# Kernel tuning notes

Hardware: AMD Instinct MI355X
Metric: run time of the kernel (lower is better)

Reference implementation:

```python
import jax, jax.numpy as jnp
import numpy as np

T, B, DIN, DH, DOUT = 512, 256, 128, 512, 128


def setup_inputs() -> dict:
    key = jax.random.key(0)
    k1, k2, k3, k4 = jax.random.split(key, 4)
    xs = jax.random.normal(k1, (T, B, DIN), dtype=jnp.float32)
    W1x = 0.1 * jax.random.normal(k2, (DIN, DH), dtype=jnp.float32)
    # random orthogonal init for the recurrent weight, as in the original
    q, _ = jnp.linalg.qr(jax.random.normal(k3, (DH, DH), dtype=jnp.float32))
    W1h = q.astype(jnp.float32)
    b1 = jnp.zeros([], dtype=jnp.float32)
    W2 = 0.1 * jax.random.normal(k4, (DH, DOUT), dtype=jnp.float32)
    b2 = jnp.zeros([], dtype=jnp.float32)
    return {"xs": xs, "W1x": W1x, "W1h": W1h, "b1": b1, "W2": W2, "b2": b2}


def reference(xs, W1x, W1h, b1, W2, b2):
    # Precompute all input projections in one big GEMM: [T, B, DH]
    xproj = jnp.einsum('tbi,ih->tbh', xs, W1x)
    h0 = jnp.zeros((xs.shape[1], W1h.shape[0]), dtype=xs.dtype)

    def step(h, xp):
        h_new = jnp.tanh(xp + h @ W1h + b1)
        return h_new, None

    h_final, _ = jax.lax.scan(step, h0, xproj)
    return h_final @ W2 + b2
```

## Files before the change

### kernel.cpp

```cpp
#include <hip/hip_runtime.h>

#define T_STEPS 512
#define BATCH   256
#define DIN     128
#define DH      512
#define DOUT    128
#define RGRP    16

typedef __attribute__((ext_vector_type(8))) short  short8;
typedef __attribute__((ext_vector_type(4))) float  floatx4;
typedef __attribute__((ext_vector_type(4))) unsigned short ushort4v;

union Pack8 { short8 s; unsigned short h[8]; };

__device__ __forceinline__ float bf2f(unsigned short u) {
    union { unsigned int i; float f; } v; v.i = ((unsigned int)u) << 16; return v.f;
}
__device__ __forceinline__ unsigned short f2bf(float f) {
    union { float f; unsigned int i; } v; v.f = f;
    unsigned int b = v.i;
    b += 0x7FFFu + ((b >> 16) & 1u);
    return (unsigned short)(b >> 16);
}
__device__ __forceinline__ float fast_tanh(float v) {
    float ex = __expf(v + v);
    return 1.f - 2.f / (ex + 1.f);
}

__global__ void pack_b_kernel(const float* __restrict__ W,
                              unsigned short* __restrict__ Wp, int K, int N) {
    int idx = blockIdx.x * blockDim.x + threadIdx.x;
    if (idx >= K * N) return;
    int k = idx / N, n = idx % N;
    int nt = n >> 4, kc = k >> 5, quad = (k >> 3) & 3, j = k & 7;
    int lane = quad * 16 + (n & 15);
    int KC = K >> 5;
    Wp[((size_t)(nt * KC + kc) * 64 + lane) * 8 + j] = f2bf(W[idx]);
}

__global__ __launch_bounds__(256) void xproj_kernel(
        const float* __restrict__ xs,
        const unsigned short* __restrict__ W1xp,
        const float* __restrict__ b1p,
        unsigned short* __restrict__ xpe) {
    const int tid  = threadIdx.x;
    const int lane = tid & 63;
    const int w    = tid >> 6;
    const int m    = lane & 15;
    const int q    = lane >> 4;
    const long row0 = (long)blockIdx.x * 16;
    const float b1 = b1p[0];

    short8 a[4];
#pragma unroll
    for (int kc = 0; kc < 4; ++kc) {
        const float* src = xs + (row0 + m) * DIN + kc * 32 + q * 8;
        Pack8 av;
#pragma unroll
        for (int j = 0; j < 8; ++j) av.h[j] = f2bf(src[j]);
        a[kc] = av.s;
    }

#pragma unroll
    for (int i = 0; i < 8; ++i) {
        const int nt = w * 8 + i;
        floatx4 acc = {0.f, 0.f, 0.f, 0.f};
#pragma unroll
        for (int kc = 0; kc < 4; ++kc) {
            short8 b = *(const short8*)(W1xp + ((size_t)(nt * 4 + kc) * 64 + lane) * 8);
            acc = __builtin_amdgcn_mfma_f32_16x16x32_bf16(a[kc], b, acc, 0, 0, 0);
        }
        ushort4v sv;
#pragma unroll
        for (int r = 0; r < 4; ++r) sv[r] = f2bf(acc[r] + b1);
        *(ushort4v*)&xpe[((size_t)blockIdx.x * 512 +
                          (size_t)(nt >> 2) * 64 + lane) * 16 + (nt & 3) * 4] = sv;
    }
}

template <int LKC>
__global__ __launch_bounds__(512) __attribute__((amdgpu_waves_per_eu(2, 2)))
void rnn_kernel(const unsigned short* __restrict__ xpe,
                const unsigned short* __restrict__ W1hp,
                const float* __restrict__ W2,
                const float* __restrict__ b2p,
                float* __restrict__ out) {
    extern __shared__ unsigned short smem[];
    unsigned short* Hb = smem;
    unsigned short* Wl = smem + 16384;

    const int tid  = threadIdx.x;
    const int lane = tid & 63;
    const int w    = tid >> 6;
    const int m    = lane & 15;
    const int q    = lane >> 4;
    const int rg   = blockIdx.x;

    constexpr int RKC  = 10;
    constexpr int SKC0 = RKC + LKC;
    constexpr int NS   = 16 - RKC - LKC;

    short8 bfr[RKC][4];
#pragma unroll
    for (int kc = 0; kc < RKC; ++kc)
#pragma unroll
        for (int i = 0; i < 4; ++i)
            bfr[kc][i] = *(const short8*)(W1hp +
                ((size_t)((4 * w + i) * 16 + kc) * 64 + lane) * 8);

    if (LKC > 0) {
        for (int c = tid; c < LKC * 2048; c += 512) {
            int j = c >> 11;
            int r2 = c & 2047;
            int nt = r2 >> 6, ln = r2 & 63;
            *(short8*)&Wl[(size_t)c * 8] =
                *(const short8*)(W1hp + ((size_t)(nt * 16 + RKC + j) * 64 + ln) * 8);
        }
    }

    const int slot = lane ^ ((lane >> 4) << 2) ^ (((lane >> 3) & 1) << 1);
    int roff = slot * 8;

    int widx[4];
#pragma unroll
    for (int i = 0; i < 4; ++i) {
        int kcp = 2 * w + (i >> 1);
        int qp  = (2 * i + (m >> 3)) & 3;
        int lp  = 4 * q + 16 * qp;
        int sl  = lp ^ ((lp >> 4) << 2) ^ (((lp >> 3) & 1) << 1);
        widx[i] = kcp * 512 + sl * 8 + (m & 7);
    }

    {
        const unsigned short* xb =
            xpe + ((size_t)rg * 512 + (size_t)w * 64 + lane) * 16;
        Pack8 x0, x1;
        x0.s = ((const short8*)xb)[0];
        x1.s = ((const short8*)xb)[1];
#pragma unroll
        for (int i = 0; i < 4; ++i) {
            Pack8 xh = (i < 2) ? x0 : x1;
#pragma unroll
            for (int r = 0; r < 4; ++r) {
                float v = bf2f(xh.h[(i & 1) * 4 + r]);
                Hb[widx[i] ^ (r << 3)] = f2bf(fast_tanh(v));
            }
            widx[i] ^= 8192;
        }
    }
    __syncthreads();

#pragma unroll 1
    for (int t = 1; t < T_STEPS; ++t) {
        asm volatile("" ::: "memory");

        const unsigned short* hrd = Hb + roff;

        short8 sb[2][4];
#pragma unroll
        for (int g = 0; g < 2; ++g)
#pragma unroll
            for (int i = 0; i < 4; ++i)
                sb[g][i] = *(const short8*)(W1hp +
                    ((size_t)((4 * w + i) * 16 + SKC0 + g) * 64 + lane) * 8);

        Pack8 x0, x1;
        {
            const unsigned short* xb = xpe +
                (((size_t)t * 16 + rg) * 512 + (size_t)w * 64 + lane) * 16;
            x0.s = ((const short8*)xb)[0];
            x1.s = ((const short8*)xb)[1];
        }

        floatx4 acc[4];
#pragma unroll
        for (int i = 0; i < 4; ++i) acc[i] = (floatx4){0.f, 0.f, 0.f, 0.f};

#pragma unroll
        for (int kc = 0; kc < RKC; ++kc) {
            short8 a = *(const short8*)&hrd[kc * 512];
#pragma unroll
            for (int i = 0; i < 4; ++i)
                acc[i] = __builtin_amdgcn_mfma_f32_16x16x32_bf16(a, bfr[kc][i], acc[i], 0, 0, 0);
        }

#pragma unroll
        for (int g = 0; g < 2; ++g) {
            short8 a = *(const short8*)&hrd[(SKC0 + g) * 512];
#pragma unroll
            for (int i = 0; i < 4; ++i)
                acc[i] = __builtin_amdgcn_mfma_f32_16x16x32_bf16(a, sb[g][i], acc[i], 0, 0, 0);
            if (g + 2 < NS) {
#pragma unroll
                for (int i = 0; i < 4; ++i)
                    sb[g][i] = *(const short8*)(W1hp +
                        ((size_t)((4 * w + i) * 16 + SKC0 + g + 2) * 64 + lane) * 8);
            }
        }

#pragma unroll
        for (int j = 0; j < LKC; ++j) {
            short8 a = *(const short8*)&hrd[(RKC + j) * 512];
#pragma unroll
            for (int i = 0; i < 4; ++i) {
                short8 b = *(const short8*)&Wl[((size_t)(j * 32 + 4 * w + i) * 64 + lane) * 8];
                acc[i] = __builtin_amdgcn_mfma_f32_16x16x32_bf16(a, b, acc[i], 0, 0, 0);
            }
        }

#pragma unroll
        for (int g = 2; g < NS; ++g) {
            short8 a = *(const short8*)&hrd[(SKC0 + g) * 512];
#pragma unroll
            for (int i = 0; i < 4; ++i)
                acc[i] = __builtin_amdgcn_mfma_f32_16x16x32_bf16(a, sb[g & 1][i], acc[i], 0, 0, 0);
            if (g + 2 < NS) {
#pragma unroll
                for (int i = 0; i < 4; ++i)
                    sb[g & 1][i] = *(const short8*)(W1hp +
                        ((size_t)((4 * w + i) * 16 + SKC0 + g + 2) * 64 + lane) * 8);
            }
        }

#pragma unroll
        for (int i = 0; i < 4; ++i) {
            Pack8 xh = (i < 2) ? x0 : x1;
#pragma unroll
            for (int r = 0; r < 4; ++r) {
                float v = acc[i][r] + bf2f(xh.h[(i & 1) * 4 + r]);
                Hb[widx[i] ^ (r << 3)] = f2bf(fast_tanh(v));
            }
            widx[i] ^= 8192;
        }
        roff ^= 8192;
        __syncthreads();
    }

    const float b2 = b2p[0];
    floatx4 acc = {0.f, 0.f, 0.f, 0.f};
#pragma unroll
    for (int kc = 0; kc < 16; ++kc) {
        short8 av = *(const short8*)&Hb[roff + kc * 512];
        Pack8 bv;
#pragma unroll
        for (int j = 0; j < 8; ++j)
            bv.h[j] = f2bf(W2[(size_t)(kc * 32 + q * 8 + j) * DOUT + w * 16 + m]);
        acc = __builtin_amdgcn_mfma_f32_16x16x32_bf16(av, bv.s, acc, 0, 0, 0);
    }
#pragma unroll
    for (int r = 0; r < 4; ++r)
        out[(size_t)(rg * 16 + q * 4 + r) * DOUT + w * 16 + m] = acc[r] + b2;
}

extern "C" void kernel_launch(void* const* d_in, const int* in_sizes, int n_in,
                              void* d_out, int out_size, void* d_ws, size_t ws_size,
                              hipStream_t stream) {
    const float* xs  = (const float*)d_in[0];
    const float* W1x = (const float*)d_in[1];
    const float* W1h = (const float*)d_in[2];
    const float* b1  = (const float*)d_in[3];
    const float* W2  = (const float*)d_in[4];
    const float* b2  = (const float*)d_in[5];
    float* out = (float*)d_out;

    unsigned short* xpe  = (unsigned short*)d_ws;
    unsigned short* w1hp = xpe + (size_t)T_STEPS * BATCH * DH;
    unsigned short* w1xp = w1hp + (size_t)DH * DH;

    pack_b_kernel<<<(DH * DH + 255) / 256, 256, 0, stream>>>(W1h, w1hp, DH, DH);
    pack_b_kernel<<<(DIN * DH + 255) / 256, 256, 0, stream>>>(W1x, w1xp, DIN, DH);
    xproj_kernel<<<(T_STEPS * BATCH) / 16, 256, 0, stream>>>(xs, w1xp, b1, xpe);

    constexpr size_t SMEM_BIG   = 32768 + 2 * 32768;
    constexpr size_t SMEM_SMALL = 32768;
    hipError_t e = hipFuncSetAttribute(
        reinterpret_cast<const void*>(&rnn_kernel<2>),
        hipFuncAttributeMaxDynamicSharedMemorySize, (int)SMEM_BIG);
    if (e == hipSuccess) {
        rnn_kernel<2><<<RGRP, 512, SMEM_BIG, stream>>>(xpe, w1hp, W2, b2, out);
    } else {
        rnn_kernel<0><<<RGRP, 512, SMEM_SMALL, stream>>>(xpe, w1hp, W2, b2, out);
    }
}
```

Before: 1.684 ms.

## Use 16 waves per block with two output tiles each for the recurrent step

Doubles the recurrent kernel's block from 512 to 1024 threads, so each wave computes 2 N-tiles of the hidden update instead of 4. This halves the MFMA chain length per wave in the serial time loop, and the fewer per-wave registers let more of W1h stay resident (8 of 16 K-chunks). The streamed W1h chunks are no longer prefetched a step ahead and are loaded just before use, which may expose global-load latency. The block barrier now covers twice as many waves.

```diff
diff --git a/kernel.cpp b/kernel.cpp
--- a/kernel.cpp
+++ b/kernel.cpp
@@ -79,12 +79,12 @@
 }
 
 template <int LKC>
-__global__ __launch_bounds__(512) __attribute__((amdgpu_waves_per_eu(2, 2)))
-void rnn_kernel(const unsigned short* __restrict__ xpe,
-                const unsigned short* __restrict__ W1hp,
-                const float* __restrict__ W2,
-                const float* __restrict__ b2p,
-                float* __restrict__ out) {
+__global__ __launch_bounds__(1024, 4)
+void rnn_kernel16(const unsigned short* __restrict__ xpe,
+                  const unsigned short* __restrict__ W1hp,
+                  const float* __restrict__ W2,
+                  const float* __restrict__ b2p,
+                  float* __restrict__ out) {
     extern __shared__ unsigned short smem[];
     unsigned short* Hb = smem;
     unsigned short* Wl = smem + 16384;
@@ -96,20 +96,21 @@
     const int q    = lane >> 4;
     const int rg   = blockIdx.x;
 
-    constexpr int RKC  = 10;
+    constexpr int RKC  = 8;
     constexpr int SKC0 = RKC + LKC;
     constexpr int NS   = 16 - RKC - LKC;
-
-    short8 bfr[RKC][4];
+    constexpr int NG   = NS / 2;
+
+    short8 bfr[RKC][2];
 #pragma unroll
     for (int kc = 0; kc < RKC; ++kc)
 #pragma unroll
-        for (int i = 0; i < 4; ++i)
+        for (int i = 0; i < 2; ++i)
             bfr[kc][i] = *(const short8*)(W1hp +
-                ((size_t)((4 * w + i) * 16 + kc) * 64 + lane) * 8);
+                ((size_t)((2 * w + i) * 16 + kc) * 64 + lane) * 8);
 
     if (LKC > 0) {
-        for (int c = tid; c < LKC * 2048; c += 512) {
+        for (int c = tid; c < LKC * 2048; c += 1024) {
             int j = c >> 11;
             int r2 = c & 2047;
             int nt = r2 >> 6, ln = r2 & 63;
@@ -121,28 +122,24 @@
     const int slot = lane ^ ((lane >> 4) << 2) ^ (((lane >> 3) & 1) << 1);
     int roff = slot * 8;
 
-    int widx[4];
-#pragma unroll
-    for (int i = 0; i < 4; ++i) {
-        int kcp = 2 * w + (i >> 1);
-        int qp  = (2 * i + (m >> 3)) & 3;
-        int lp  = 4 * q + 16 * qp;
-        int sl  = lp ^ ((lp >> 4) << 2) ^ (((lp >> 3) & 1) << 1);
-        widx[i] = kcp * 512 + sl * 8 + (m & 7);
+    int widx[2];
+#pragma unroll
+    for (int i = 0; i < 2; ++i) {
+        int qp = 2 * i + (m >> 3);
+        int lp = 16 * qp + 4 * q;
+        int sl = lp ^ ((lp >> 4) << 2) ^ (((lp >> 3) & 1) << 1);
+        widx[i] = w * 512 + sl * 8 + (m & 7);
     }
 
     {
-        const unsigned short* xb =
-            xpe + ((size_t)rg * 512 + (size_t)w * 64 + lane) * 16;
-        Pack8 x0, x1;
-        x0.s = ((const short8*)xb)[0];
-        x1.s = ((const short8*)xb)[1];
-#pragma unroll
-        for (int i = 0; i < 4; ++i) {
-            Pack8 xh = (i < 2) ? x0 : x1;
+        const unsigned short* xb = xpe +
+            ((size_t)rg * 512 + (size_t)(w >> 1) * 64 + lane) * 16 + (w & 1) * 8;
+        Pack8 x0; x0.s = *(const short8*)xb;
+#pragma unroll
+        for (int i = 0; i < 2; ++i) {
 #pragma unroll
             for (int r = 0; r < 4; ++r) {
-                float v = bf2f(xh.h[(i & 1) * 4 + r]);
+                float v = bf2f(x0.h[i * 4 + r]);
                 Hb[widx[i] ^ (r << 3)] = f2bf(fast_tanh(v));
             }
             widx[i] ^= 8192;
@@ -156,78 +153,56 @@
 
         const unsigned short* hrd = Hb + roff;
 
-        short8 sb[2][4];
-#pragma unroll
-        for (int g = 0; g < 2; ++g)
-#pragma unroll
-            for (int i = 0; i < 4; ++i)
-                sb[g][i] = *(const short8*)(W1hp +
-                    ((size_t)((4 * w + i) * 16 + SKC0 + g) * 64 + lane) * 8);
-
-        Pack8 x0, x1;
-        {
-            const unsigned short* xb = xpe +
-                (((size_t)t * 16 + rg) * 512 + (size_t)w * 64 + lane) * 16;
-            x0.s = ((const short8*)xb)[0];
-            x1.s = ((const short8*)xb)[1];
-        }
-
-        floatx4 acc[4];
-#pragma unroll
-        for (int i = 0; i < 4; ++i) acc[i] = (floatx4){0.f, 0.f, 0.f, 0.f};
+        Pack8 xh;
+        xh.s = *(const short8*)(xpe +
+            (((size_t)t * 16 + rg) * 512 + (size_t)(w >> 1) * 64 + lane) * 16 +
+            (w & 1) * 8);
+
+        floatx4 acc[2];
+#pragma unroll
+        for (int i = 0; i < 2; ++i) acc[i] = (floatx4){0.f, 0.f, 0.f, 0.f};
 
 #pragma unroll
         for (int kc = 0; kc < RKC; ++kc) {
             short8 a = *(const short8*)&hrd[kc * 512];
 #pragma unroll
-            for (int i = 0; i < 4; ++i)
+            for (int i = 0; i < 2; ++i)
                 acc[i] = __builtin_amdgcn_mfma_f32_16x16x32_bf16(a, bfr[kc][i], acc[i], 0, 0, 0);
-        }
-
-#pragma unroll
-        for (int g = 0; g < 2; ++g) {
-            short8 a = *(const short8*)&hrd[(SKC0 + g) * 512];
-#pragma unroll
-            for (int i = 0; i < 4; ++i)
-                acc[i] = __builtin_amdgcn_mfma_f32_16x16x32_bf16(a, sb[g][i], acc[i], 0, 0, 0);
-            if (g + 2 < NS) {
-#pragma unroll
-                for (int i = 0; i < 4; ++i)
-                    sb[g][i] = *(const short8*)(W1hp +
-                        ((size_t)((4 * w + i) * 16 + SKC0 + g + 2) * 64 + lane) * 8);
-            }
         }
 
 #pragma unroll
         for (int j = 0; j < LKC; ++j) {
             short8 a = *(const short8*)&hrd[(RKC + j) * 512];
 #pragma unroll
-            for (int i = 0; i < 4; ++i) {
-                short8 b = *(const short8*)&Wl[((size_t)(j * 32 + 4 * w + i) * 64 + lane) * 8];
+            for (int i = 0; i < 2; ++i) {
+                short8 b = *(const short8*)&Wl[((size_t)(j * 32 + 2 * w + i) * 64 + lane) * 8];
                 acc[i] = __builtin_amdgcn_mfma_f32_16x16x32_bf16(a, b, acc[i], 0, 0, 0);
             }
         }
 
 #pragma unroll
-        for (int g = 2; g < NS; ++g) {
-            short8 a = *(const short8*)&hrd[(SKC0 + g) * 512];
-#pragma unroll
-            for (int i = 0; i < 4; ++i)
-                acc[i] = __builtin_amdgcn_mfma_f32_16x16x32_bf16(a, sb[g & 1][i], acc[i], 0, 0, 0);
-            if (g + 2 < NS) {
-#pragma unroll
-                for (int i = 0; i < 4; ++i)
-                    sb[g & 1][i] = *(const short8*)(W1hp +
-                        ((size_t)((4 * w + i) * 16 + SKC0 + g + 2) * 64 + lane) * 8);
-            }
-        }
-
-#pragma unroll
-        for (int i = 0; i < 4; ++i) {
-            Pack8 xh = (i < 2) ? x0 : x1;
+        for (int g = 0; g < NG; ++g) {
+            short8 sb[2][2];
+#pragma unroll
+            for (int c = 0; c < 2; ++c)
+#pragma unroll
+                for (int i = 0; i < 2; ++i)
+                    sb[c][i] = *(const short8*)(W1hp +
+                        ((size_t)((2 * w + i) * 16 + SKC0 + 2 * g + c) * 64 + lane) * 8);
+#pragma unroll
+            for (int c = 0; c < 2; ++c) {
+                short8 a = *(const short8*)&hrd[(SKC0 + 2 * g + c) * 512];
+#pragma unroll
+                for (int i = 0; i < 2; ++i)
+                    acc[i] = __builtin_amdgcn_mfma_f32_16x16x32_bf16(a, sb[c][i], acc[i], 0, 0, 0);
+            }
+        }
+
+#pragma unroll
+        for (int i = 0; i < 2; ++i) {
 #pragma unroll
             for (int r = 0; r < 4; ++r) {
-                float v = acc[i][r] + bf2f(xh.h[(i & 1) * 4 + r]);
+                float v = acc[i][r] + bf2f(xh.h[i * 4 + r]);
                 Hb[widx[i] ^ (r << 3)] = f2bf(fast_tanh(v));
             }
             widx[i] ^= 8192;
@@ -236,20 +211,22 @@
         __syncthreads();
     }
 
-    const float b2 = b2p[0];
-    floatx4 acc = {0.f, 0.f, 0.f, 0.f};
-#pragma unroll
-    for (int kc = 0; kc < 16; ++kc) {
-        short8 av = *(const short8*)&Hb[roff + kc * 512];
-        Pack8 bv;
-#pragma unroll
-        for (int j = 0; j < 8; ++j)
-            bv.h[j] = f2bf(W2[(size_t)(kc * 32 + q * 8 + j) * DOUT + w * 16 + m]);
-        acc = __builtin_amdgcn_mfma_f32_16x16x32_bf16(av, bv.s, acc, 0, 0, 0);
-    }
-#pragma unroll
-    for (int r = 0; r < 4; ++r)
-        out[(size_t)(rg * 16 + q * 4 + r) * DOUT + w * 16 + m] = acc[r] + b2;
+    if (w < 8) {
+        const float b2 = b2p[0];
+        floatx4 acc = {0.f, 0.f, 0.f, 0.f};
+#pragma unroll
+        for (int kc = 0; kc < 16; ++kc) {
+            short8 av = *(const short8*)&Hb[roff + kc * 512];
+            Pack8 bv;
+#pragma unroll
+            for (int j = 0; j < 8; ++j)
+                bv.h[j] = f2bf(W2[(size_t)(kc * 32 + q * 8 + j) * DOUT + w * 16 + m]);
+            acc = __builtin_amdgcn_mfma_f32_16x16x32_bf16(av, bv.s, acc, 0, 0, 0);
+        }
+#pragma unroll
+        for (int r = 0; r < 4; ++r)
+            out[(size_t)(rg * 16 + q * 4 + r) * DOUT + w * 16 + m] = acc[r] + b2;
+    }
 }
 
 extern "C" void kernel_launch(void* const* d_in, const int* in_sizes, int n_in,
@@ -274,11 +251,11 @@
     constexpr size_t SMEM_BIG   = 32768 + 2 * 32768;
     constexpr size_t SMEM_SMALL = 32768;
     hipError_t e = hipFuncSetAttribute(
-        reinterpret_cast<const void*>(&rnn_kernel<2>),
+        reinterpret_cast<const void*>(&rnn_kernel16<2>),
         hipFuncAttributeMaxDynamicSharedMemorySize, (int)SMEM_BIG);
     if (e == hipSuccess) {
-        rnn_kernel<2><<<RGRP, 512, SMEM_BIG, stream>>>(xpe, w1hp, W2, b2, out);
+        rnn_kernel16<2><<<RGRP, 1024, SMEM_BIG, stream>>>(xpe, w1hp, W2, b2, out);
     } else {
-        rnn_kernel<0><<<RGRP, 512, SMEM_SMALL, stream>>>(xpe, w1hp, W2, b2, out);
-    }
-}
+        rnn_kernel16<0><<<RGRP, 1024, SMEM_SMALL, stream>>>(xpe, w1hp, W2, b2, out);
+    }
+}
```

After: 1.881 ms. 1.12x slower.

## Pin resident W1h fragments in AGPRs and stage more chunks in LDS

Applied to the files above, without the earlier changes.

The recurrent kernel now keeps the register-resident W1h fragments in accumulator registers (AGPRs) by way of inline asm constraints, and feeds them straight to inline MFMA instructions. The register-resident K chunks drop from 10 to 8, and LDS-staged chunks rise from 2 to 4 (160KB LDS). The remaining streamed chunks are loaded two at a time, with the LDS chunks placed between the streamed groups. The aim is to relieve VGPR pressure and cut per-step global weight traffic, at the cost of heavy LDS use, and the inline asm may hide hazards from the compiler's scheduler.

```diff
diff --git a/kernel.cpp b/kernel.cpp
--- a/kernel.cpp
+++ b/kernel.cpp
@@ -80,11 +80,11 @@
 
 template <int LKC>
 __global__ __launch_bounds__(512) __attribute__((amdgpu_waves_per_eu(2, 2)))
-void rnn_kernel(const unsigned short* __restrict__ xpe,
-                const unsigned short* __restrict__ W1hp,
-                const float* __restrict__ W2,
-                const float* __restrict__ b2p,
-                float* __restrict__ out) {
+void rnn_agpr(const unsigned short* __restrict__ xpe,
+              const unsigned short* __restrict__ W1hp,
+              const float* __restrict__ W2,
+              const float* __restrict__ b2p,
+              float* __restrict__ out) {
     extern __shared__ unsigned short smem[];
     unsigned short* Hb = smem;
     unsigned short* Wl = smem + 16384;
@@ -96,17 +96,20 @@
     const int q    = lane >> 4;
     const int rg   = blockIdx.x;
 
-    constexpr int RKC  = 10;
+    constexpr int RKC  = 8;
     constexpr int SKC0 = RKC + LKC;
     constexpr int NS   = 16 - RKC - LKC;
-
-    short8 bfr[RKC][4];
+    constexpr int NG   = NS / 2;
+
+    short8 wa[RKC][4];
 #pragma unroll
     for (int kc = 0; kc < RKC; ++kc)
 #pragma unroll
-        for (int i = 0; i < 4; ++i)
-            bfr[kc][i] = *(const short8*)(W1hp +
+        for (int i = 0; i < 4; ++i) {
+            wa[kc][i] = *(const short8*)(W1hp +
                 ((size_t)((4 * w + i) * 16 + kc) * 64 + lane) * 8);
+            asm("" : "+a"(wa[kc][i]));
+        }
 
     if (LKC > 0) {
         for (int c = tid; c < LKC * 2048; c += 512) {
@@ -158,11 +161,11 @@
 
         short8 sb[2][4];
 #pragma unroll
-        for (int g = 0; g < 2; ++g)
+        for (int c = 0; c < 2; ++c)
 #pragma unroll
             for (int i = 0; i < 4; ++i)
-                sb[g][i] = *(const short8*)(W1hp +
-                    ((size_t)((4 * w + i) * 16 + SKC0 + g) * 64 + lane) * 8);
+                sb[c][i] = *(const short8*)(W1hp +
+                    ((size_t)((4 * w + i) * 16 + SKC0 + c) * 64 + lane) * 8);
 
         Pack8 x0, x1;
         {
@@ -181,44 +184,37 @@
             short8 a = *(const short8*)&hrd[kc * 512];
 #pragma unroll
             for (int i = 0; i < 4; ++i)
-                acc[i] = __builtin_amdgcn_mfma_f32_16x16x32_bf16(a, bfr[kc][i], acc[i], 0, 0, 0);
-        }
-
-#pragma unroll
-        for (int g = 0; g < 2; ++g) {
-            short8 a = *(const short8*)&hrd[(SKC0 + g) * 512];
-#pragma unroll
-            for (int i = 0; i < 4; ++i)
-                acc[i] = __builtin_amdgcn_mfma_f32_16x16x32_bf16(a, sb[g][i], acc[i], 0, 0, 0);
-            if (g + 2 < NS) {
+                asm("v_mfma_f32_16x16x32_bf16 %0, %1, %2, %0"
+                    : "+v"(acc[i]) : "v"(a), "a"(wa[kc][i]));
+        }
+
+#pragma unroll
+        for (int g = 0; g < NG; ++g) {
+#pragma unroll
+            for (int c = 0; c < 2; ++c) {
+                short8 a = *(const short8*)&hrd[(SKC0 + 2 * g + c) * 512];
 #pragma unroll
                 for (int i = 0; i < 4; ++i)
-                    sb[g][i] = *(const short8*)(W1hp +
-                        ((size_t)((4 * w + i) * 16 + SKC0 + g + 2) * 64 + lane) * 8);
-            }
-        }
-
-#pragma unroll
-        for (int j = 0; j < LKC; ++j) {
-            short8 a = *(const short8*)&hrd[(RKC + j) * 512];
-#pragma unroll
-            for (int i = 0; i < 4; ++i) {
-                short8 b = *(const short8*)&Wl[((size_t)(j * 32 + 4 * w + i) * 64 + lane) * 8];
-                acc[i] = __builtin_amdgcn_mfma_f32_16x16x32_bf16(a, b, acc[i], 0, 0, 0);
-            }
-        }
-
-#pragma unroll
-        for (int g = 2; g < NS; ++g) {
-            short8 a = *(const short8*)&hrd[(SKC0 + g) * 512];
-#pragma unroll
-            for (int i = 0; i < 4; ++i)
-                acc[i] = __builtin_amdgcn_mfma_f32_16x16x32_bf16(a, sb[g & 1][i], acc[i], 0, 0, 0);
-            if (g + 2 < NS) {
-#pragma unroll
-                for (int i = 0; i < 4; ++i)
-                    sb[g & 1][i] = *(const short8*)(W1hp +
-                        ((size_t)((4 * w + i) * 16 + SKC0 + g + 2) * 64 + lane) * 8);
+                    acc[i] = __builtin_amdgcn_mfma_f32_16x16x32_bf16(a, sb[c][i], acc[i], 0, 0, 0);
+            }
+            if (g + 1 < NG) {
+#pragma unroll
+                for (int c = 0; c < 2; ++c)
+#pragma unroll
+                    for (int i = 0; i < 4; ++i)
+                        sb[c][i] = *(const short8*)(W1hp +
+                            ((size_t)((4 * w + i) * 16 + SKC0 + 2 * (g + 1) + c) * 64 + lane) * 8);
+            }
+            if (g == 0 && LKC > 0) {
+#pragma unroll
+                for (int j = 0; j < LKC; ++j) {
+                    short8 a = *(const short8*)&hrd[(RKC + j) * 512];
+#pragma unroll
+                    for (int i = 0; i < 4; ++i) {
+                        short8 b = *(const short8*)&Wl[((size_t)(j * 32 + 4 * w + i) * 64 + lane) * 8];
+                        acc[i] = __builtin_amdgcn_mfma_f32_16x16x32_bf16(a, b, acc[i], 0, 0, 0);
+                    }
+                }
             }
         }
 
@@ -271,14 +267,14 @@
     pack_b_kernel<<<(DIN * DH + 255) / 256, 256, 0, stream>>>(W1x, w1xp, DIN, DH);
     xproj_kernel<<<(T_STEPS * BATCH) / 16, 256, 0, stream>>>(xs, w1xp, b1, xpe);
 
-    constexpr size_t SMEM_BIG   = 32768 + 2 * 32768;
+    constexpr size_t SMEM_BIG   = 32768 + 4 * 32768;
     constexpr size_t SMEM_SMALL = 32768;
     hipError_t e = hipFuncSetAttribute(
-        reinterpret_cast<const void*>(&rnn_kernel<2>),
+        reinterpret_cast<const void*>(&rnn_agpr<4>),
         hipFuncAttributeMaxDynamicSharedMemorySize, (int)SMEM_BIG);
     if (e == hipSuccess) {
-        rnn_kernel<2><<<RGRP, 512, SMEM_BIG, stream>>>(xpe, w1hp, W2, b2, out);
+        rnn_agpr<4><<<RGRP, 512, SMEM_BIG, stream>>>(xpe, w1hp, W2, b2, out);
     } else {
-        rnn_kernel<0><<<RGRP, 512, SMEM_SMALL, stream>>>(xpe, w1hp, W2, b2, out);
-    }
-}
+        rnn_agpr<0><<<RGRP, 512, SMEM_SMALL, stream>>>(xpe, w1hp, W2, b2, out);
+    }
+}
```

Measured after the change: 1.825 ms. +8.4%, slower.
